# Kernel optimization log

Measured on AMD Instinct MI355X. Metric: run time of the kernel, lower is better.

The kernel has to match this reference:

```python
import jax, jax.numpy as jnp
import numpy as np

N_NODES = 200000
N_RELS = 500
ENT_DIM = 128
REL_DIM = 128
B = 500000


def _xavier(key, shape):
    # xavier_uniform_ for a (num_emb, dim) matrix: bound = sqrt(6/(fan_in+fan_out))
    bound = np.sqrt(6.0 / (shape[0] + shape[1])).astype(np.float32)
    return jax.random.uniform(key, shape, jnp.float32, -bound, bound)


def setup_inputs() -> dict:
    key = jax.random.key(0)
    ks = jax.random.split(key, 9)
    return {
        "head_emb": _xavier(ks[0], (N_NODES, ENT_DIM)),
        "head_emb_p": _xavier(ks[1], (N_NODES, ENT_DIM)),
        "tail_emb": _xavier(ks[2], (N_NODES, ENT_DIM)),
        "tail_emb_p": _xavier(ks[3], (N_NODES, ENT_DIM)),
        "rel_emb": _xavier(ks[4], (N_RELS, REL_DIM)),
        "rel_emb_p": _xavier(ks[5], (N_RELS, REL_DIM)),
        "head_indices": jax.random.randint(ks[6], (B,), 0, N_NODES),
        "tail_indices": jax.random.randint(ks[7], (B,), 0, N_NODES),
        "relation_indices": jax.random.randint(ks[8], (B,), 0, N_RELS),
    }


def reference(head_emb, head_emb_p, tail_emb, tail_emb_p, rel_emb, rel_emb_p,
              head_indices, tail_indices, relation_indices):
    # Gather embeddings
    h = head_emb[head_indices]          # [B, De]
    h_p = head_emb_p[head_indices]      # [B, De]
    t = tail_emb[tail_indices]          # [B, De]
    t_p = tail_emb_p[tail_indices]      # [B, De]
    r = rel_emb[relation_indices]       # [B, Dr]
    r_p = rel_emb_p[relation_indices]   # [B, Dr]

    # (r_p h_p^T + 1) h  ==  r_p * (h_p . h) + sum(h)   (rank-1 + all-ones matrix)
    head_proj = r_p * jnp.sum(h_p * h, axis=-1, keepdims=True) + jnp.sum(h, axis=-1, keepdims=True)
    tail_proj = r_p * jnp.sum(t_p * t, axis=-1, keepdims=True) + jnp.sum(t, axis=-1, keepdims=True)

    diff = head_proj + r - tail_proj    # [B, Dr]
    scores = jnp.sum(diff * diff, axis=-1)  # ||.||_2^2
    return scores
```

## Files before the change

kernel.cpp:

```cpp
#include <hip/hip_runtime.h>
#include <hip/hip_bf16.h>


#define ENT_DIM 128

__global__ void node_stats_kernel(const float* __restrict__ he,
                                  const float* __restrict__ hep,
                                  const float* __restrict__ te,
                                  const float* __restrict__ tep,
                                  float2* __restrict__ hstats,
                                  float2* __restrict__ tstats,
                                  int n_nodes) {
    const int wave  = (blockIdx.x * blockDim.x + threadIdx.x) >> 6;
    const int lane  = threadIdx.x & 63;
    const int sub   = lane >> 3;
    const int chunk = lane & 7;
    const int njobs = 2 * n_nodes;

    const int job = wave * 8 + sub;
    if (job >= njobs) return;

    const bool is_head = job < n_nodes;
    const int node = is_head ? job : job - n_nodes;
    const float* emb  = is_head ? he  : te;
    const float* embp = is_head ? hep : tep;
    float2* st = is_head ? hstats : tstats;

    const float4* pe  = (const float4*)(emb  + (size_t)node * ENT_DIM) + chunk;
    const float4* pep = (const float4*)(embp + (size_t)node * ENT_DIM) + chunk;

    float4 v[4], vp[4];
    #pragma unroll
    for (int k = 0; k < 4; ++k) v[k]  = pe[k * 8];
    #pragma unroll
    for (int k = 0; k < 4; ++k) vp[k] = pep[k * 8];

    float s = 0.0f, d = 0.0f;
    #pragma unroll
    for (int k = 0; k < 4; ++k) {
        s += (v[k].x + v[k].y) + (v[k].z + v[k].w);
        d += v[k].x * vp[k].x + v[k].y * vp[k].y
           + v[k].z * vp[k].z + v[k].w * vp[k].w;
    }
    #pragma unroll
    for (int off = 4; off >= 1; off >>= 1) {
        s += __shfl_xor(s, off, 64);
        d += __shfl_xor(d, off, 64);
    }
    if (chunk == 0) st[node] = make_float2(s, d);
}

__global__ void rel_stats_kernel(const float* __restrict__ re,
                                 const float* __restrict__ rep,
                                 float* __restrict__ rstats, int n_rels) {
    const int wave = (blockIdx.x * blockDim.x + threadIdx.x) >> 6;
    const int lane = threadIdx.x & 63;
    if (wave >= n_rels) return;

    const float2 r = ((const float2*)(re  + (size_t)wave * ENT_DIM))[lane];
    const float2 p = ((const float2*)(rep + (size_t)wave * ENT_DIM))[lane];
    float s_pp = p.x * p.x + p.y * p.y;
    float s_p  = p.x + p.y;
    float s_pr = p.x * r.x + p.y * r.y;
    float s_r  = r.x + r.y;
    float s_rr = r.x * r.x + r.y * r.y;
    #pragma unroll
    for (int off = 32; off >= 1; off >>= 1) {
        s_pp += __shfl_xor(s_pp, off, 64);
        s_p  += __shfl_xor(s_p,  off, 64);
        s_pr += __shfl_xor(s_pr, off, 64);
        s_r  += __shfl_xor(s_r,  off, 64);
        s_rr += __shfl_xor(s_rr, off, 64);
    }
    if (lane == 0) {
        float* o = rstats + (size_t)wave * 8;
        o[0] = s_pp; o[1] = s_p; o[2] = s_pr; o[3] = s_r; o[4] = s_rr;
    }
}

__global__ void score_kernel(const int* __restrict__ hidx,
                             const int* __restrict__ tidx,
                             const int* __restrict__ ridx,
                             const float2* __restrict__ hstats,
                             const float2* __restrict__ tstats,
                             const float* __restrict__ rstats,
                             float* __restrict__ out, int B) {
    const int t = blockIdx.x * blockDim.x + threadIdx.x;
    const int T = gridDim.x * blockDim.x;

    int hi[4], ti[4], ri[4];
    bool act[4];
    #pragma unroll
    for (int u = 0; u < 4; ++u) {
        const int b = t + u * T;
        act[u] = b < B;
        if (act[u]) { hi[u] = hidx[b]; ti[u] = tidx[b]; ri[u] = ridx[b]; }
    }
    float2 hs[4], ts[4];
    float4 q0[4];
    float  q4[4];
    #pragma unroll
    for (int u = 0; u < 4; ++u) {
        if (act[u]) {
            hs[u] = hstats[hi[u]];
            ts[u] = tstats[ti[u]];
            const float* q = rstats + (size_t)ri[u] * 8;
            q0[u] = *(const float4*)q;
            q4[u] = q[4];
        }
    }
    #pragma unroll
    for (int u = 0; u < 4; ++u) {
        if (act[u]) {
            const int b = t + u * T;
            const float c = hs[u].x - ts[u].x;
            const float a = hs[u].y - ts[u].y;
            out[b] = a * a * q0[u].x + c * c * (float)ENT_DIM + q4[u]
                   + 2.0f * (a * c * q0[u].y + a * q0[u].z + c * q0[u].w);
        }
    }
}

__global__ void direct_kernel(const float* __restrict__ he, const float* __restrict__ hep,
                              const float* __restrict__ te, const float* __restrict__ tep,
                              const float* __restrict__ re, const float* __restrict__ rep,
                              const int* __restrict__ hidx, const int* __restrict__ tidx,
                              const int* __restrict__ ridx,
                              float* __restrict__ out, int B) {
    const int wave = (blockIdx.x * blockDim.x + threadIdx.x) >> 6;
    const int lane = threadIdx.x & 63;
    if (wave >= B) return;
    const int hi = hidx[wave], ti = tidx[wave], ri = ridx[wave];
    const float2 h  = ((const float2*)(he  + (size_t)hi * ENT_DIM))[lane];
    const float2 hp = ((const float2*)(hep + (size_t)hi * ENT_DIM))[lane];
    const float2 t  = ((const float2*)(te  + (size_t)ti * ENT_DIM))[lane];
    const float2 tp = ((const float2*)(tep + (size_t)ti * ENT_DIM))[lane];
    const float2 r  = ((const float2*)(re  + (size_t)ri * ENT_DIM))[lane];
    const float2 rp = ((const float2*)(rep + (size_t)ri * ENT_DIM))[lane];
    float hd = h.x * hp.x + h.y * hp.y;
    float hs = h.x + h.y;
    float td = t.x * tp.x + t.y * tp.y;
    float ts = t.x + t.y;
    #pragma unroll
    for (int off = 32; off >= 1; off >>= 1) {
        hd += __shfl_xor(hd, off, 64);
        hs += __shfl_xor(hs, off, 64);
        td += __shfl_xor(td, off, 64);
        ts += __shfl_xor(ts, off, 64);
    }
    const float a = hd - td, c = hs - ts;
    const float dx = a * rp.x + c + r.x;
    const float dy = a * rp.y + c + r.y;
    float sc = dx * dx + dy * dy;
    #pragma unroll
    for (int off = 32; off >= 1; off >>= 1) sc += __shfl_xor(sc, off, 64);
    if (lane == 0) out[wave] = sc;
}

extern "C" void kernel_launch(void* const* d_in, const int* in_sizes, int n_in,
                              void* d_out, int out_size, void* d_ws, size_t ws_size,
                              hipStream_t stream) {
    const float* he  = (const float*)d_in[0];
    const float* hep = (const float*)d_in[1];
    const float* te  = (const float*)d_in[2];
    const float* tep = (const float*)d_in[3];
    const float* re  = (const float*)d_in[4];
    const float* rep = (const float*)d_in[5];
    const int* hidx  = (const int*)d_in[6];
    const int* tidx  = (const int*)d_in[7];
    const int* ridx  = (const int*)d_in[8];
    float* out = (float*)d_out;

    const int n_nodes = in_sizes[0] / ENT_DIM;
    const int n_rels  = in_sizes[4] / ENT_DIM;
    const int B       = in_sizes[6];

    const size_t hstats_bytes = (size_t)n_nodes * sizeof(float2);
    const size_t rstats_bytes = (size_t)n_rels * 8 * sizeof(float);
    const size_t need = 2 * hstats_bytes + rstats_bytes;

    if (ws_size >= need) {
        float2* hstats = (float2*)d_ws;
        float2* tstats = (float2*)((char*)d_ws + hstats_bytes);
        float*  rstats = (float*)((char*)d_ws + 2 * hstats_bytes);

        const int njobs   = 2 * n_nodes;
        const int waves1  = (njobs + 7) / 8;
        const int blocks1 = (waves1 + 3) / 4;
        node_stats_kernel<<<blocks1, 256, 0, stream>>>(he, hep, te, tep,
                                                       hstats, tstats, n_nodes);
        const int blocks2 = (n_rels * 64 + 255) / 256;
        rel_stats_kernel<<<blocks2, 256, 0, stream>>>(re, rep, rstats, n_rels);
        const int threads3 = (B + 3) / 4;
        const int blocks3  = (threads3 + 255) / 256;
        score_kernel<<<blocks3, 256, 0, stream>>>(hidx, tidx, ridx,
                                                  hstats, tstats, rstats, out, B);
    } else {
        const int blocks = (B * 64 + 255) / 256;
        direct_kernel<<<blocks, 256, 0, stream>>>(he, hep, te, tep, re, rep,
                                                  hidx, tidx, ridx, out, B);
    }
}
```

Measured before the change: 359.3 us.

## Make node stats kernel persistent with software-pipelined prefetch of next batch

Replaces the one-shot node statistics kernel with a persistent grid of 1024 blocks. Each wave grid-strides over batches of 8 rows, prefetching the next batch's embeddings into registers while reducing the current one. Each half-wave now handles a full row with contiguous float4 loads, and the reductions use 5-step shuffles over 32 lanes. The aim is to keep more loads in flight and cut launch and tail overhead on a bandwidth-bound pass over about 400 MB. In exchange, register use goes up and the fixed grid size may not fill the GPU or hide latency as well as the original oversubscribed launch.

```diff
diff --git a/kernel.cpp b/kernel.cpp
--- a/kernel.cpp
+++ b/kernel.cpp
@@ -4,50 +4,86 @@
 
 #define ENT_DIM 128
 
-__global__ void node_stats_kernel(const float* __restrict__ he,
-                                  const float* __restrict__ hep,
-                                  const float* __restrict__ te,
-                                  const float* __restrict__ tep,
-                                  float2* __restrict__ hstats,
-                                  float2* __restrict__ tstats,
-                                  int n_nodes) {
-    const int wave  = (blockIdx.x * blockDim.x + threadIdx.x) >> 6;
-    const int lane  = threadIdx.x & 63;
-    const int sub   = lane >> 3;
-    const int chunk = lane & 7;
-    const int njobs = 2 * n_nodes;
-
-    const int job = wave * 8 + sub;
-    if (job >= njobs) return;
-
-    const bool is_head = job < n_nodes;
-    const int node = is_head ? job : job - n_nodes;
-    const float* emb  = is_head ? he  : te;
-    const float* embp = is_head ? hep : tep;
-    float2* st = is_head ? hstats : tstats;
-
-    const float4* pe  = (const float4*)(emb  + (size_t)node * ENT_DIM) + chunk;
-    const float4* pep = (const float4*)(embp + (size_t)node * ENT_DIM) + chunk;
-
-    float4 v[4], vp[4];
-    #pragma unroll
-    for (int k = 0; k < 4; ++k) v[k]  = pe[k * 8];
-    #pragma unroll
-    for (int k = 0; k < 4; ++k) vp[k] = pep[k * 8];
-
-    float s = 0.0f, d = 0.0f;
-    #pragma unroll
-    for (int k = 0; k < 4; ++k) {
-        s += (v[k].x + v[k].y) + (v[k].z + v[k].w);
-        d += v[k].x * vp[k].x + v[k].y * vp[k].y
-           + v[k].z * vp[k].z + v[k].w * vp[k].w;
-    }
-    #pragma unroll
-    for (int off = 4; off >= 1; off >>= 1) {
-        s += __shfl_xor(s, off, 64);
-        d += __shfl_xor(d, off, 64);
-    }
-    if (chunk == 0) st[node] = make_float2(s, d);
+__device__ __forceinline__ void nsk_load_batch(
+        const float* __restrict__ he, const float* __restrict__ hep,
+        const float* __restrict__ te, const float* __restrict__ tep,
+        int n_nodes, int b, int half, int l,
+        float4 v[4], float4 vp[4]) {
+    #pragma unroll
+    for (int i = 0; i < 4; ++i) {
+        const int row = 8 * b + 2 * i + half;
+        const bool is_head = row < n_nodes;
+        const int node = is_head ? row : row - n_nodes;
+        const float* e  = is_head ? he  : te;
+        const float* ep = is_head ? hep : tep;
+        v[i]  = ((const float4*)(e  + (size_t)node * ENT_DIM))[l];
+        vp[i] = ((const float4*)(ep + (size_t)node * ENT_DIM))[l];
+    }
+}
+
+__device__ __forceinline__ void nsk_process_batch(
+        float2* __restrict__ hstats, float2* __restrict__ tstats,
+        int n_nodes, int b, int half, int l,
+        const float4 v[4], const float4 vp[4]) {
+    float s[4], d[4];
+    #pragma unroll
+    for (int i = 0; i < 4; ++i) {
+        s[i] = (v[i].x + v[i].y) + (v[i].z + v[i].w);
+        d[i] = v[i].x * vp[i].x + v[i].y * vp[i].y
+             + v[i].z * vp[i].z + v[i].w * vp[i].w;
+    }
+    #pragma unroll
+    for (int off = 16; off >= 1; off >>= 1) {
+        #pragma unroll
+        for (int i = 0; i < 4; ++i) {
+            s[i] += __shfl_xor(s[i], off, 64);
+            d[i] += __shfl_xor(d[i], off, 64);
+        }
+    }
+    if (l == 0) {
+        #pragma unroll
+        for (int i = 0; i < 4; ++i) {
+            const int row = 8 * b + 2 * i + half;
+            const bool is_head = row < n_nodes;
+            const int node = is_head ? row : row - n_nodes;
+            float2* st = is_head ? hstats : tstats;
+            st[node] = make_float2(s[i], d[i]);
+        }
+    }
+}
+
+__global__ void __launch_bounds__(256, 4)
+node_stats_kernel(const float* __restrict__ he,
+                  const float* __restrict__ hep,
+                  const float* __restrict__ te,
+                  const float* __restrict__ tep,
+                  float2* __restrict__ hstats,
+                  float2* __restrict__ tstats,
+                  int n_nodes) {
+    const int wid  = (blockIdx.x * blockDim.x + threadIdx.x) >> 6;
+    const int nw   = (gridDim.x * blockDim.x) >> 6;
+    const int lane = threadIdx.x & 63;
+    const int half = lane >> 5;
+    const int l    = lane & 31;
+    const int NB   = (2 * n_nodes + 7) / 8;
+
+    int b = wid;
+    if (b >= NB) return;
+
+    float4 cv[4], cp[4];
+    nsk_load_batch(he, hep, te, tep, n_nodes, b, half, l, cv, cp);
+
+    while (true) {
+        const int nb = b + nw;
+        float4 nv[4], np_[4];
+        if (nb < NB)
+            nsk_load_batch(he, hep, te, tep, n_nodes, nb, half, l, nv, np_);
+        nsk_process_batch(hstats, tstats, n_nodes, b, half, l, cv, cp);
+        if (nb >= NB) break;
+        #pragma unroll
+        for (int i = 0; i < 4; ++i) { cv[i] = nv[i]; cp[i] = np_[i]; }
+        b = nb;
+    }
 }
 
 __global__ void rel_stats_kernel(const float* __restrict__ re,
@@ -184,11 +220,8 @@
         float2* tstats = (float2*)((char*)d_ws + hstats_bytes);
         float*  rstats = (float*)((char*)d_ws + 2 * hstats_bytes);
 
-        const int njobs   = 2 * n_nodes;
-        const int waves1  = (njobs + 7) / 8;
-        const int blocks1 = (waves1 + 3) / 4;
-        node_stats_kernel<<<blocks1, 256, 0, stream>>>(he, hep, te, tep,
-                                                       hstats, tstats, n_nodes);
+        node_stats_kernel<<<1024, 256, 0, stream>>>(he, hep, te, tep,
+                                                    hstats, tstats, n_nodes);
         const int blocks2 = (n_rels * 64 + 255) / 256;
         rel_stats_kernel<<<blocks2, 256, 0, stream>>>(re, rep, rstats, n_rels);
         const int threads3 = (B + 3) / 4;
```

New measurement: 362.1 us. No clear change (+0.8%).
